# Kernel tuning notes

Hardware: AMD Instinct MI355X
Metric: run time of the kernel (lower is better)

The kernel has to match this reference:

```python
import jax, jax.numpy as jnp
import numpy as np

H = 8           # num_heads
TANH_CLIP = 10.0


def setup_inputs() -> dict:
    key = jax.random.key(0)
    ks = jax.random.split(key, 7)
    B, N, D = 512, 1000, 128
    embeddings = jax.random.normal(ks[0], (B, N, D), dtype=jnp.float32)
    context_feat = jax.random.normal(ks[1], (B, 2 * D), dtype=jnp.float32)
    W_node = jax.random.normal(ks[2], (D, 3 * D), dtype=jnp.float32) / np.sqrt(D)
    W_fixed = jax.random.normal(ks[3], (D, D), dtype=jnp.float32) / np.sqrt(D)
    W_step = jax.random.normal(ks[4], (2 * D, D), dtype=jnp.float32) / np.sqrt(2 * D)
    W_out = jax.random.normal(ks[5], (D, D), dtype=jnp.float32) / np.sqrt(D)
    # action_mask: True = feasible node; ensure at least one feasible per row
    action_mask = jax.random.uniform(ks[6], (B, N)) > 0.3
    action_mask = action_mask.at[:, 0].set(True)
    return {"embeddings": embeddings, "context_feat": context_feat,
            "W_node": W_node, "W_fixed": W_fixed, "W_step": W_step,
            "W_out": W_out, "action_mask": action_mask}


def reference(embeddings, context_feat, W_node, W_fixed, W_step, W_out, action_mask):
    B, N, D = embeddings.shape
    dk = D // H
    # --- _precompute ---
    graph_context = (embeddings.mean(axis=1) @ W_fixed)[:, None, :]      # [B,1,D]
    proj = embeddings @ W_node                                            # [B,N,3D]
    gk, gv, logit_k = jnp.split(proj, 3, axis=-1)                         # each [B,N,D]
    to_heads = lambda x: x.reshape(B, N, H, dk).transpose(2, 0, 1, 3)     # [H,B,N,dk]
    K, V = to_heads(gk), to_heads(gv)
    # --- _get_log_p: query (num_steps = 1) ---
    q = graph_context + (context_feat @ W_step)[:, None, :]               # [B,1,D]
    Q = q.reshape(B, 1, H, dk).transpose(2, 0, 1, 3)                      # [H,B,1,dk]
    mask = ~action_mask                                                    # [B,N], True = infeasible
    # --- glimpse attention (mask_inner) ---
    compat = jnp.einsum('hbqd,hbnd->hbqn', Q, K) / jnp.sqrt(jnp.asarray(dk, Q.dtype))
    compat = jnp.where(mask[None, :, None, :], -jnp.inf, compat)
    attn = jax.nn.softmax(compat, axis=-1)                                 # [H,B,1,N]
    heads = jnp.einsum('hbqn,hbnd->hbqd', attn, V)                         # [H,B,1,dk]
    glimpse = heads.transpose(1, 2, 0, 3).reshape(B, 1, D) @ W_out         # [B,1,D]
    # --- tanh-clipped single-head logits ---
    logits = jnp.einsum('bqd,bnd->bqn', glimpse, logit_k) / jnp.sqrt(jnp.asarray(D, glimpse.dtype))
    logits = jnp.tanh(logits) * TANH_CLIP
    logits = jnp.where(mask[:, None, :], -jnp.inf, logits)                 # [B,1,N]
    return logits
```

## Files before the change

### kernel.cpp

```cpp
#include <hip/hip_runtime.h>
#include <math.h>

#define BB 512
#define NN 1000
#define DD 128
#define HH 8
#define TILE 125

#define WS_AFOLD 4096

__device__ __forceinline__ bool mask_feasible(const void* mask, int flag, int idx) {
    if (flag == 1) return ((const int*)mask)[idx] != 0;
    if (flag == 2) return ((const float*)mask)[idx] != 0.0f;
    return ((const unsigned char*)mask)[idx] != 0;
}

__device__ __forceinline__ float rdl(float v, int srclane) {
    return __int_as_float(__builtin_amdgcn_readlane(__float_as_int(v), srclane));
}

__global__ void k0_detect(const unsigned int* __restrict__ m, int* __restrict__ flag) {
    int t = threadIdx.x;
    unsigned int w = m[t];
    unsigned long long bi = __ballot(w <= 1u);
    unsigned long long bf = __ballot(w == 0u || w == 0x3F800000u);
    if (t == 0) {
        int f = 0;
        if (bi == ~0ull) f = 1;
        else if (bf == ~0ull) f = 2;
        *flag = f;
    }
}

__global__ __launch_bounds__(512) void kA_meanfold(
    const float* __restrict__ emb, const float* __restrict__ ctx,
    const float* __restrict__ W_fixed, const float* __restrict__ W_step,
    const float* __restrict__ W_node, float* __restrict__ Afold) {
    int b = blockIdx.x, t = threadIdx.x;
    __shared__ float4 red[512];
    __shared__ float mean_s[DD], cld[2 * DD], qlds[DD];
    int q4 = t & 31, j = t >> 5;
    const float4* e4 = (const float4*)(emb + (size_t)b * NN * DD);
    float4 acc = {0.f, 0.f, 0.f, 0.f};
    for (int n = j; n < NN; n += 16) {
        float4 v = e4[n * 32 + q4];
        acc.x += v.x; acc.y += v.y; acc.z += v.z; acc.w += v.w;
    }
    red[t] = acc;
    __syncthreads();
    for (int s = 8; s >= 1; s >>= 1) {
        if (j < s) {
            float4 o = red[t + s * 32], m = red[t];
            m.x += o.x; m.y += o.y; m.z += o.z; m.w += o.w;
            red[t] = m;
        }
        __syncthreads();
    }
    if (t < 32) {
        float4 m = red[t];
        const float inv = 1.0f / (float)NN;
        float4 r = {m.x * inv, m.y * inv, m.z * inv, m.w * inv};
        ((float4*)mean_s)[t] = r;
    }
    if (t < 256) cld[t] = ctx[b * 2 * DD + t];
    __syncthreads();
    if (t < 128) {
        float a = 0.f;
        for (int c = 0; c < DD; ++c)     a += mean_s[c] * W_fixed[c * DD + t];
        for (int c = 0; c < 2 * DD; ++c) a += cld[c] * W_step[c * DD + t];
        qlds[t] = a;
    }
    __syncthreads();
    if (t < 128) {
        int c = t;
        const float* wrow = W_node + (size_t)c * 3 * DD;
        float* Ab = Afold + (size_t)b * 1024;
        for (int h = 0; h < HH; ++h) {
            float a = 0.f;
#pragma unroll
            for (int d0 = 0; d0 < 16; ++d0) a += wrow[h * 16 + d0] * qlds[h * 16 + d0];
            Ab[c * 8 + h] = 0.25f * a;
        }
    }
}

__global__ __launch_bounds__(256) void kB_flash(
    const float* __restrict__ emb, const float* __restrict__ Afold,
    const void* __restrict__ mask, const int* __restrict__ flagp,
    const float* __restrict__ W_node, const float* __restrict__ W_out,
    float* __restrict__ out) {
    int b = blockIdx.x, t = threadIdx.x;
    int flag = *flagp;
    int wave = t >> 6, lane = t & 63;
    int hq = (t >> 7) * 4;
    int n = t & 127;
    int c4 = t & 31, jr = t >> 5;

    __shared__ float4 tile4[128][32];
    __shared__ float cbuf[128][8];
    __shared__ float wemb_s[8][128];
    __shared__ float mrun[8], zrun[8], scale_s[8], mnew_s[8];
    __shared__ float4 wmax4[4];
    __shared__ float4 zstage[4][2];
    __shared__ float hl[DD];
    __shared__ float4 gl4[32];

    const float* Ab = Afold + (size_t)b * 1024;
    float a0l = Ab[lane * 8 + hq + 0], a1l = Ab[lane * 8 + hq + 1];
    float a2l = Ab[lane * 8 + hq + 2], a3l = Ab[lane * 8 + hq + 3];
    float a0h = Ab[(64 + lane) * 8 + hq + 0], a1h = Ab[(64 + lane) * 8 + hq + 1];
    float a2h = Ab[(64 + lane) * 8 + hq + 2], a3h = Ab[(64 + lane) * 8 + hq + 3];

    float4 wacc[8];
#pragma unroll
    for (int h = 0; h < HH; ++h) wacc[h] = make_float4(0.f, 0.f, 0.f, 0.f);
    if (t < 8) { mrun[t] = -INFINITY; zrun[t] = 0.f; }
    __syncthreads();

    const float4* embB4 = (const float4*)(emb + (size_t)b * NN * DD);
    const int mbase = b * NN;

    for (int tile = 0; tile < 8; ++tile) {
        int n0 = tile * TILE;
#pragma unroll
        for (int idx = 0; idx < 16; ++idx) {
            int i = t + idx * 256;
            if (i < TILE * 32) {
                int r = i >> 5, c = i & 31;
                tile4[r][c ^ (r & 31)] = embB4[n0 * 32 + i];
            }
        }
        __syncthreads();
        float4 cv = make_float4(-INFINITY, -INFINITY, -INFINITY, -INFINITY);
        if (n < TILE) {
            int sw = n & 31;
            float4 s = make_float4(0.f, 0.f, 0.f, 0.f);
#pragma unroll 4
            for (int k = 0; k < 16; ++k) {
                float4 e = tile4[n][k ^ sw];
                int c = k * 4;
                s.x += e.x * rdl(a0l, c) + e.y * rdl(a0l, c + 1) + e.z * rdl(a0l, c + 2) + e.w * rdl(a0l, c + 3);
                s.y += e.x * rdl(a1l, c) + e.y * rdl(a1l, c + 1) + e.z * rdl(a1l, c + 2) + e.w * rdl(a1l, c + 3);
                s.z += e.x * rdl(a2l, c) + e.y * rdl(a2l, c + 1) + e.z * rdl(a2l, c + 2) + e.w * rdl(a2l, c + 3);
                s.w += e.x * rdl(a3l, c) + e.y * rdl(a3l, c + 1) + e.z * rdl(a3l, c + 2) + e.w * rdl(a3l, c + 3);
            }
#pragma unroll 4
            for (int k = 16; k < 32; ++k) {
                float4 e = tile4[n][k ^ sw];
                int c = k * 4 - 64;
                s.x += e.x * rdl(a0h, c) + e.y * rdl(a0h, c + 1) + e.z * rdl(a0h, c + 2) + e.w * rdl(a0h, c + 3);
                s.y += e.x * rdl(a1h, c) + e.y * rdl(a1h, c + 1) + e.z * rdl(a1h, c + 2) + e.w * rdl(a1h, c + 3);
                s.z += e.x * rdl(a2h, c) + e.y * rdl(a2h, c + 1) + e.z * rdl(a2h, c + 2) + e.w * rdl(a2h, c + 3);
                s.w += e.x * rdl(a3h, c) + e.y * rdl(a3h, c + 1) + e.z * rdl(a3h, c + 2) + e.w * rdl(a3h, c + 3);
            }
            if (mask_feasible(mask, flag, mbase + n0 + n)) cv = s;
            *(float4*)&cbuf[n][hq] = cv;
        }
        {
            float4 wm = cv;
#pragma unroll
            for (int off = 1; off < 64; off <<= 1) {
                wm.x = fmaxf(wm.x, __shfl_xor(wm.x, off));
                wm.y = fmaxf(wm.y, __shfl_xor(wm.y, off));
                wm.z = fmaxf(wm.z, __shfl_xor(wm.z, off));
                wm.w = fmaxf(wm.w, __shfl_xor(wm.w, off));
            }
            if (lane == 0) wmax4[wave] = wm;
        }
        __syncthreads();
        if (t < 8) {
            int w0 = (t < 4) ? 0 : 2, hi = t & 3;
            float m = fmaxf(((float*)&wmax4[w0])[hi], ((float*)&wmax4[w0 + 1])[hi]);
            float mold = mrun[t];
            float mn = fmaxf(mold, m);
            mnew_s[t] = mn;
            scale_s[t] = (mn == -INFINITY) ? 1.0f : __expf(mold - mn);
            mrun[t] = mn;
        }
        __syncthreads();
        {
            float m0 = mnew_s[hq], m1 = mnew_s[hq + 1], m2 = mnew_s[hq + 2], m3 = mnew_s[hq + 3];
            float4 p = make_float4(0.f, 0.f, 0.f, 0.f);
            if (n < TILE) {
                p.x = (cv.x == -INFINITY) ? 0.f : __expf(cv.x - m0);
                p.y = (cv.y == -INFINITY) ? 0.f : __expf(cv.y - m1);
                p.z = (cv.z == -INFINITY) ? 0.f : __expf(cv.z - m2);
                p.w = (cv.w == -INFINITY) ? 0.f : __expf(cv.w - m3);
                *(float4*)&cbuf[n][hq] = p;
            }
#pragma unroll
            for (int off = 1; off < 64; off <<= 1) {
                p.x += __shfl_xor(p.x, off);
                p.y += __shfl_xor(p.y, off);
                p.z += __shfl_xor(p.z, off);
                p.w += __shfl_xor(p.w, off);
            }
            if (lane == 0) zstage[wave][hq >> 2] = p;
            float sc0 = scale_s[0], sc1 = scale_s[1], sc2 = scale_s[2], sc3 = scale_s[3];
            float sc4 = scale_s[4], sc5 = scale_s[5], sc6 = scale_s[6], sc7 = scale_s[7];
            wacc[0].x *= sc0; wacc[0].y *= sc0; wacc[0].z *= sc0; wacc[0].w *= sc0;
            wacc[1].x *= sc1; wacc[1].y *= sc1; wacc[1].z *= sc1; wacc[1].w *= sc1;
            wacc[2].x *= sc2; wacc[2].y *= sc2; wacc[2].z *= sc2; wacc[2].w *= sc2;
            wacc[3].x *= sc3; wacc[3].y *= sc3; wacc[3].z *= sc3; wacc[3].w *= sc3;
            wacc[4].x *= sc4; wacc[4].y *= sc4; wacc[4].z *= sc4; wacc[4].w *= sc4;
            wacc[5].x *= sc5; wacc[5].y *= sc5; wacc[5].z *= sc5; wacc[5].w *= sc5;
            wacc[6].x *= sc6; wacc[6].y *= sc6; wacc[6].z *= sc6; wacc[6].w *= sc6;
            wacc[7].x *= sc7; wacc[7].y *= sc7; wacc[7].z *= sc7; wacc[7].w *= sc7;
        }
        __syncthreads();
        if (t < 8) {
            int w0 = (t < 4) ? 0 : 2;
            float zn = ((float*)&zstage[w0][t >> 2])[t & 3] + ((float*)&zstage[w0 + 1][t >> 2])[t & 3];
            zrun[t] = zrun[t] * scale_s[t] + zn;
        }
        for (int nn = jr; nn < TILE; nn += 8) {
            float4 e = tile4[nn][c4 ^ (nn & 31)];
            float4 pA = *(const float4*)&cbuf[nn][0];
            float4 pB = *(const float4*)&cbuf[nn][4];
            wacc[0].x += pA.x * e.x; wacc[0].y += pA.x * e.y; wacc[0].z += pA.x * e.z; wacc[0].w += pA.x * e.w;
            wacc[1].x += pA.y * e.x; wacc[1].y += pA.y * e.y; wacc[1].z += pA.y * e.z; wacc[1].w += pA.y * e.w;
            wacc[2].x += pA.z * e.x; wacc[2].y += pA.z * e.y; wacc[2].z += pA.z * e.z; wacc[2].w += pA.z * e.w;
            wacc[3].x += pA.w * e.x; wacc[3].y += pA.w * e.y; wacc[3].z += pA.w * e.z; wacc[3].w += pA.w * e.w;
            wacc[4].x += pB.x * e.x; wacc[4].y += pB.x * e.y; wacc[4].z += pB.x * e.z; wacc[4].w += pB.x * e.w;
            wacc[5].x += pB.y * e.x; wacc[5].y += pB.y * e.y; wacc[5].z += pB.y * e.z; wacc[5].w += pB.y * e.w;
            wacc[6].x += pB.z * e.x; wacc[6].y += pB.z * e.y; wacc[6].z += pB.z * e.z; wacc[6].w += pB.z * e.w;
            wacc[7].x += pB.w * e.x; wacc[7].y += pB.w * e.y; wacc[7].z += pB.w * e.z; wacc[7].w += pB.w * e.w;
        }
        __syncthreads();
    }
    {
        float4* red = (float4*)&tile4[0][0];
#pragma unroll
        for (int h = 0; h < HH; ++h) red[(jr * 32 + c4) * 8 + h] = wacc[h];
        __syncthreads();
        int cc = t >> 3, hh = t & 7;
        float4 s = make_float4(0.f, 0.f, 0.f, 0.f);
#pragma unroll
        for (int jj = 0; jj < 8; ++jj) {
            float4 v = red[(jj * 32 + cc) * 8 + hh];
            s.x += v.x; s.y += v.y; s.z += v.z; s.w += v.w;
        }
        float inv = 1.0f / zrun[hh];
        s.x *= inv; s.y *= inv; s.z *= inv; s.w *= inv;
        *(float4*)&wemb_s[hh][cc * 4] = s;
    }
    __syncthreads();
    if (t < 128) {
        int h = t >> 4;
        float a = 0.f;
        for (int c = 0; c < DD; ++c) a += wemb_s[h][c] * W_node[(size_t)c * 384 + 128 + t];
        hl[t] = a;
    }
    __syncthreads();
    if (t < 128) {
        float g = 0.f;
        for (int k = 0; k < DD; ++k) g += hl[k] * W_out[k * DD + t];
        ((float*)gl4)[t] = g;
    }
    __syncthreads();
    if (t < 128) {
        float a3 = 0.f;
        const float* wr = W_node + (size_t)t * 384 + 256;
        const float* glp = (const float*)gl4;
        for (int d = 0; d < DD; ++d) a3 += wr[d] * glp[d];
        hl[t] = a3;
    }
    __syncthreads();
    const float4* g2v = (const float4*)hl;
    for (int r = t; r < NN; r += 256) {
        const float4* row = embB4 + (size_t)r * 32;
        float acc = 0.f;
#pragma unroll 8
        for (int k = 0; k < 32; ++k) {
            float4 e = row[k], g = g2v[k];
            acc += e.x * g.x + e.y * g.y + e.z * g.z + e.w * g.w;
        }
        bool feas = mask_feasible(mask, flag, mbase + r);
        out[(size_t)mbase + r] = feas ? (10.0f * tanhf(acc * 0.08838834764831845f)) : -1.0e30f;
    }
}

extern "C" void kernel_launch(void* const* d_in, const int* in_sizes, int n_in,
                              void* d_out, int out_size, void* d_ws, size_t ws_size,
                              hipStream_t stream) {
    (void)in_sizes; (void)n_in; (void)out_size; (void)ws_size;
    const float* emb     = (const float*)d_in[0];
    const float* ctx     = (const float*)d_in[1];
    const float* W_node  = (const float*)d_in[2];
    const float* W_fixed = (const float*)d_in[3];
    const float* W_step  = (const float*)d_in[4];
    const float* W_out   = (const float*)d_in[5];
    const void*  mask    = d_in[6];
    float* out = (float*)d_out;

    char* ws = (char*)d_ws;
    int*   flag  = (int*)(ws + 0);
    float* Afold = (float*)(ws + WS_AFOLD);

    k0_detect<<<1, 64, 0, stream>>>((const unsigned int*)mask, flag);
    kA_meanfold<<<BB, 512, 0, stream>>>(emb, ctx, W_fixed, W_step, W_node, Afold);
    kB_flash<<<BB, 256, 0, stream>>>(emb, Afold, mask, flag, W_node, W_out, out);
}
```

Measured before the change: 200.6 us.

## Fuse mean/fold kernel into flash kernel and widen block to 512 threads

Merges the per-batch mean/query-fold kernel into the attention kernel, so the folded query matrix stays in shared memory instead of going through a workspace. The block grows to 512 threads with each thread computing 2 heads instead of 4, and cbuf is transposed to a head-major layout. This removes one launch and a global round trip, and puts more waves on each batch row. The cost is that the embedding mean pass now runs inside the same block ahead of the tile loop, and register pressure with the 8 float4 accumulators at 512 threads may limit occupancy.

```diff
diff --git a/kernel.cpp b/kernel.cpp
--- a/kernel.cpp
+++ b/kernel.cpp
@@ -6,8 +6,6 @@
 #define DD 128
 #define HH 8
 #define TILE 125
-
-#define WS_AFOLD 4096
 
 __device__ __forceinline__ bool mask_feasible(const void* mask, int flag, int idx) {
     if (flag == 1) return ((const int*)mask)[idx] != 0;
@@ -32,145 +30,126 @@
     }
 }
 
-__global__ __launch_bounds__(512) void kA_meanfold(
+__global__ __launch_bounds__(512, 4) void kMega(
     const float* __restrict__ emb, const float* __restrict__ ctx,
     const float* __restrict__ W_fixed, const float* __restrict__ W_step,
-    const float* __restrict__ W_node, float* __restrict__ Afold) {
-    int b = blockIdx.x, t = threadIdx.x;
-    __shared__ float4 red[512];
-    __shared__ float mean_s[DD], cld[2 * DD], qlds[DD];
-    int q4 = t & 31, j = t >> 5;
-    const float4* e4 = (const float4*)(emb + (size_t)b * NN * DD);
-    float4 acc = {0.f, 0.f, 0.f, 0.f};
-    for (int n = j; n < NN; n += 16) {
-        float4 v = e4[n * 32 + q4];
-        acc.x += v.x; acc.y += v.y; acc.z += v.z; acc.w += v.w;
-    }
-    red[t] = acc;
-    __syncthreads();
-    for (int s = 8; s >= 1; s >>= 1) {
-        if (j < s) {
-            float4 o = red[t + s * 32], m = red[t];
-            m.x += o.x; m.y += o.y; m.z += o.z; m.w += o.w;
-            red[t] = m;
-        }
-        __syncthreads();
-    }
-    if (t < 32) {
-        float4 m = red[t];
-        const float inv = 1.0f / (float)NN;
-        float4 r = {m.x * inv, m.y * inv, m.z * inv, m.w * inv};
-        ((float4*)mean_s)[t] = r;
-    }
-    if (t < 256) cld[t] = ctx[b * 2 * DD + t];
-    __syncthreads();
-    if (t < 128) {
-        float a = 0.f;
-        for (int c = 0; c < DD; ++c)     a += mean_s[c] * W_fixed[c * DD + t];
-        for (int c = 0; c < 2 * DD; ++c) a += cld[c] * W_step[c * DD + t];
-        qlds[t] = a;
-    }
-    __syncthreads();
-    if (t < 128) {
-        int c = t;
-        const float* wrow = W_node + (size_t)c * 3 * DD;
-        float* Ab = Afold + (size_t)b * 1024;
-        for (int h = 0; h < HH; ++h) {
-            float a = 0.f;
-#pragma unroll
-            for (int d0 = 0; d0 < 16; ++d0) a += wrow[h * 16 + d0] * qlds[h * 16 + d0];
-            Ab[c * 8 + h] = 0.25f * a;
-        }
-    }
-}
-
-__global__ __launch_bounds__(256) void kB_flash(
-    const float* __restrict__ emb, const float* __restrict__ Afold,
+    const float* __restrict__ W_node, const float* __restrict__ W_out,
     const void* __restrict__ mask, const int* __restrict__ flagp,
-    const float* __restrict__ W_node, const float* __restrict__ W_out,
     float* __restrict__ out) {
     int b = blockIdx.x, t = threadIdx.x;
     int flag = *flagp;
     int wave = t >> 6, lane = t & 63;
-    int hq = (t >> 7) * 4;
+    int hq = (t >> 7) * 2;
     int n = t & 127;
     int c4 = t & 31, jr = t >> 5;
 
     __shared__ float4 tile4[128][32];
-    __shared__ float cbuf[128][8];
-    __shared__ float wemb_s[8][128];
+    __shared__ float cbuf[HH][DD];
+    __shared__ float small[1536];
     __shared__ float mrun[8], zrun[8], scale_s[8], mnew_s[8];
-    __shared__ float4 wmax4[4];
-    __shared__ float4 zstage[4][2];
-    __shared__ float hl[DD];
-    __shared__ float4 gl4[32];
-
-    const float* Ab = Afold + (size_t)b * 1024;
-    float a0l = Ab[lane * 8 + hq + 0], a1l = Ab[lane * 8 + hq + 1];
-    float a2l = Ab[lane * 8 + hq + 2], a3l = Ab[lane * 8 + hq + 3];
-    float a0h = Ab[(64 + lane) * 8 + hq + 0], a1h = Ab[(64 + lane) * 8 + hq + 1];
-    float a2h = Ab[(64 + lane) * 8 + hq + 2], a3h = Ab[(64 + lane) * 8 + hq + 3];
-
-    float4 wacc[8];
-#pragma unroll
-    for (int h = 0; h < HH; ++h) wacc[h] = make_float4(0.f, 0.f, 0.f, 0.f);
-    if (t < 8) { mrun[t] = -INFINITY; zrun[t] = 0.f; }
-    __syncthreads();
+    __shared__ float2 wmax2[8], zstage[8];
 
     const float4* embB4 = (const float4*)(emb + (size_t)b * NN * DD);
     const int mbase = b * NN;
 
+    {
+        float4 acc = make_float4(0.f, 0.f, 0.f, 0.f);
+        for (int nn = jr; nn < NN; nn += 16) {
+            float4 v = embB4[nn * 32 + c4];
+            acc.x += v.x; acc.y += v.y; acc.z += v.z; acc.w += v.w;
+        }
+        float4* red = (float4*)tile4;
+        red[t] = acc;
+        __syncthreads();
+        for (int s = 8; s >= 1; s >>= 1) {
+            if (jr < s) {
+                float4 o = red[t + s * 32], m = red[t];
+                m.x += o.x; m.y += o.y; m.z += o.z; m.w += o.w;
+                red[t] = m;
+            }
+            __syncthreads();
+        }
+        if (t < 32) {
+            float4 m = red[t];
+            const float inv = 1.0f / (float)NN;
+            float4 r = {m.x * inv, m.y * inv, m.z * inv, m.w * inv};
+            ((float4*)&small[0])[t] = r;
+        }
+        if (t >= 256) small[t] = ctx[b * 2 * DD + (t - 256)];
+    }
+    __syncthreads();
+    if (t < 128) {
+        float a = 0.f;
+        for (int c = 0; c < DD; ++c)     a += small[c] * W_fixed[c * DD + t];
+        for (int c = 0; c < 2 * DD; ++c) a += small[256 + c] * W_step[c * DD + t];
+        small[128 + t] = a;
+    }
+    __syncthreads();
+    if (t < 128) {
+        const float* wrow = W_node + (size_t)t * 384;
+        for (int h = 0; h < HH; ++h) {
+            float a = 0.f;
+#pragma unroll
+            for (int d0 = 0; d0 < 16; ++d0) a += wrow[h * 16 + d0] * small[128 + h * 16 + d0];
+            small[512 + t * 8 + h] = 0.25f * a;
+        }
+    }
+    if (t < 8) { mrun[t] = -INFINITY; zrun[t] = 0.f; }
+    __syncthreads();
+    float a0l = small[512 + lane * 8 + hq],        a1l = small[512 + lane * 8 + hq + 1];
+    float a0h = small[512 + (64 + lane) * 8 + hq], a1h = small[512 + (64 + lane) * 8 + hq + 1];
+
+    float4 wacc[8];
+#pragma unroll
+    for (int h = 0; h < HH; ++h) wacc[h] = make_float4(0.f, 0.f, 0.f, 0.f);
+
     for (int tile = 0; tile < 8; ++tile) {
         int n0 = tile * TILE;
 #pragma unroll
-        for (int idx = 0; idx < 16; ++idx) {
-            int i = t + idx * 256;
+        for (int idx = 0; idx < 8; ++idx) {
+            int i = t + idx * 512;
             if (i < TILE * 32) {
                 int r = i >> 5, c = i & 31;
                 tile4[r][c ^ (r & 31)] = embB4[n0 * 32 + i];
             }
         }
         __syncthreads();
-        float4 cv = make_float4(-INFINITY, -INFINITY, -INFINITY, -INFINITY);
+        float2 cv = make_float2(-INFINITY, -INFINITY);
         if (n < TILE) {
             int sw = n & 31;
-            float4 s = make_float4(0.f, 0.f, 0.f, 0.f);
-#pragma unroll 4
+            float sx = 0.f, sy = 0.f;
+#pragma unroll
             for (int k = 0; k < 16; ++k) {
                 float4 e = tile4[n][k ^ sw];
                 int c = k * 4;
-                s.x += e.x * rdl(a0l, c) + e.y * rdl(a0l, c + 1) + e.z * rdl(a0l, c + 2) + e.w * rdl(a0l, c + 3);
-                s.y += e.x * rdl(a1l, c) + e.y * rdl(a1l, c + 1) + e.z * rdl(a1l, c + 2) + e.w * rdl(a1l, c + 3);
-                s.z += e.x * rdl(a2l, c) + e.y * rdl(a2l, c + 1) + e.z * rdl(a2l, c + 2) + e.w * rdl(a2l, c + 3);
-                s.w += e.x * rdl(a3l, c) + e.y * rdl(a3l, c + 1) + e.z * rdl(a3l, c + 2) + e.w * rdl(a3l, c + 3);
-            }
-#pragma unroll 4
+                sx += e.x * rdl(a0l, c) + e.y * rdl(a0l, c + 1) + e.z * rdl(a0l, c + 2) + e.w * rdl(a0l, c + 3);
+                sy += e.x * rdl(a1l, c) + e.y * rdl(a1l, c + 1) + e.z * rdl(a1l, c + 2) + e.w * rdl(a1l, c + 3);
+            }
+#pragma unroll
             for (int k = 16; k < 32; ++k) {
                 float4 e = tile4[n][k ^ sw];
                 int c = k * 4 - 64;
-                s.x += e.x * rdl(a0h, c) + e.y * rdl(a0h, c + 1) + e.z * rdl(a0h, c + 2) + e.w * rdl(a0h, c + 3);
-                s.y += e.x * rdl(a1h, c) + e.y * rdl(a1h, c + 1) + e.z * rdl(a1h, c + 2) + e.w * rdl(a1h, c + 3);
-                s.z += e.x * rdl(a2h, c) + e.y * rdl(a2h, c + 1) + e.z * rdl(a2h, c + 2) + e.w * rdl(a2h, c + 3);
-                s.w += e.x * rdl(a3h, c) + e.y * rdl(a3h, c + 1) + e.z * rdl(a3h, c + 2) + e.w * rdl(a3h, c + 3);
-            }
-            if (mask_feasible(mask, flag, mbase + n0 + n)) cv = s;
-            *(float4*)&cbuf[n][hq] = cv;
+                sx += e.x * rdl(a0h, c) + e.y * rdl(a0h, c + 1) + e.z * rdl(a0h, c + 2) + e.w * rdl(a0h, c + 3);
+                sy += e.x * rdl(a1h, c) + e.y * rdl(a1h, c + 1) + e.z * rdl(a1h, c + 2) + e.w * rdl(a1h, c + 3);
+            }
+            if (mask_feasible(mask, flag, mbase + n0 + n)) { cv.x = sx; cv.y = sy; }
+            cbuf[hq][n] = cv.x;
+            cbuf[hq + 1][n] = cv.y;
         }
         {
-            float4 wm = cv;
+            float2 wm = cv;
 #pragma unroll
             for (int off = 1; off < 64; off <<= 1) {
                 wm.x = fmaxf(wm.x, __shfl_xor(wm.x, off));
                 wm.y = fmaxf(wm.y, __shfl_xor(wm.y, off));
-                wm.z = fmaxf(wm.z, __shfl_xor(wm.z, off));
-                wm.w = fmaxf(wm.w, __shfl_xor(wm.w, off));
-            }
-            if (lane == 0) wmax4[wave] = wm;
+            }
+            if (lane == 0) wmax2[wave] = wm;
         }
         __syncthreads();
         if (t < 8) {
-            int w0 = (t < 4) ? 0 : 2, hi = t & 3;
-            float m = fmaxf(((float*)&wmax4[w0])[hi], ((float*)&wmax4[w0 + 1])[hi]);
+            int w0 = (t >> 1) * 2;
+            float m = (t & 1) ? fmaxf(wmax2[w0].y, wmax2[w0 + 1].y)
+                              : fmaxf(wmax2[w0].x, wmax2[w0 + 1].x);
             float mold = mrun[t];
             float mn = fmaxf(mold, m);
             mnew_s[t] = mn;
@@ -179,23 +158,20 @@
         }
         __syncthreads();
         {
-            float m0 = mnew_s[hq], m1 = mnew_s[hq + 1], m2 = mnew_s[hq + 2], m3 = mnew_s[hq + 3];
-            float4 p = make_float4(0.f, 0.f, 0.f, 0.f);
+            float m0 = mnew_s[hq], m1 = mnew_s[hq + 1];
+            float2 p = make_float2(0.f, 0.f);
             if (n < TILE) {
                 p.x = (cv.x == -INFINITY) ? 0.f : __expf(cv.x - m0);
                 p.y = (cv.y == -INFINITY) ? 0.f : __expf(cv.y - m1);
-                p.z = (cv.z == -INFINITY) ? 0.f : __expf(cv.z - m2);
-                p.w = (cv.w == -INFINITY) ? 0.f : __expf(cv.w - m3);
-                *(float4*)&cbuf[n][hq] = p;
+                cbuf[hq][n] = p.x;
+                cbuf[hq + 1][n] = p.y;
             }
 #pragma unroll
             for (int off = 1; off < 64; off <<= 1) {
                 p.x += __shfl_xor(p.x, off);
                 p.y += __shfl_xor(p.y, off);
-                p.z += __shfl_xor(p.z, off);
-                p.w += __shfl_xor(p.w, off);
-            }
-            if (lane == 0) zstage[wave][hq >> 2] = p;
+            }
+            if (lane == 0) zstage[wave] = p;
             float sc0 = scale_s[0], sc1 = scale_s[1], sc2 = scale_s[2], sc3 = scale_s[3];
             float sc4 = scale_s[4], sc5 = scale_s[5], sc6 = scale_s[6], sc7 = scale_s[7];
             wacc[0].x *= sc0; wacc[0].y *= sc0; wacc[0].z *= sc0; wacc[0].w *= sc0;
@@ -209,65 +185,67 @@
         }
         __syncthreads();
         if (t < 8) {
-            int w0 = (t < 4) ? 0 : 2;
-            float zn = ((float*)&zstage[w0][t >> 2])[t & 3] + ((float*)&zstage[w0 + 1][t >> 2])[t & 3];
+            int w0 = (t >> 1) * 2;
+            float zn = (t & 1) ? (zstage[w0].y + zstage[w0 + 1].y)
+                               : (zstage[w0].x + zstage[w0 + 1].x);
             zrun[t] = zrun[t] * scale_s[t] + zn;
         }
-        for (int nn = jr; nn < TILE; nn += 8) {
+        for (int nn = jr; nn < TILE; nn += 16) {
             float4 e = tile4[nn][c4 ^ (nn & 31)];
-            float4 pA = *(const float4*)&cbuf[nn][0];
-            float4 pB = *(const float4*)&cbuf[nn][4];
-            wacc[0].x += pA.x * e.x; wacc[0].y += pA.x * e.y; wacc[0].z += pA.x * e.z; wacc[0].w += pA.x * e.w;
-            wacc[1].x += pA.y * e.x; wacc[1].y += pA.y * e.y; wacc[1].z += pA.y * e.z; wacc[1].w += pA.y * e.w;
-            wacc[2].x += pA.z * e.x; wacc[2].y += pA.z * e.y; wacc[2].z += pA.z * e.z; wacc[2].w += pA.z * e.w;
-            wacc[3].x += pA.w * e.x; wacc[3].y += pA.w * e.y; wacc[3].z += pA.w * e.z; wacc[3].w += pA.w * e.w;
-            wacc[4].x += pB.x * e.x; wacc[4].y += pB.x * e.y; wacc[4].z += pB.x * e.z; wacc[4].w += pB.x * e.w;
-            wacc[5].x += pB.y * e.x; wacc[5].y += pB.y * e.y; wacc[5].z += pB.y * e.z; wacc[5].w += pB.y * e.w;
-            wacc[6].x += pB.z * e.x; wacc[6].y += pB.z * e.y; wacc[6].z += pB.z * e.z; wacc[6].w += pB.z * e.w;
-            wacc[7].x += pB.w * e.x; wacc[7].y += pB.w * e.y; wacc[7].z += pB.w * e.z; wacc[7].w += pB.w * e.w;
+            float p0 = cbuf[0][nn], p1 = cbuf[1][nn], p2 = cbuf[2][nn], p3 = cbuf[3][nn];
+            float p4 = cbuf[4][nn], p5 = cbuf[5][nn], p6 = cbuf[6][nn], p7 = cbuf[7][nn];
+            wacc[0].x += p0 * e.x; wacc[0].y += p0 * e.y; wacc[0].z += p0 * e.z; wacc[0].w += p0 * e.w;
+            wacc[1].x += p1 * e.x; wacc[1].y += p1 * e.y; wacc[1].z += p1 * e.z; wacc[1].w += p1 * e.w;
+            wacc[2].x += p2 * e.x; wacc[2].y += p2 * e.y; wacc[2].z += p2 * e.z; wacc[2].w += p2 * e.w;
+            wacc[3].x += p3 * e.x; wacc[3].y += p3 * e.y; wacc[3].z += p3 * e.z; wacc[3].w += p3 * e.w;
+            wacc[4].x += p4 * e.x; wacc[4].y += p4 * e.y; wacc[4].z += p4 * e.z; wacc[4].w += p4 * e.w;
+            wacc[5].x += p5 * e.x; wacc[5].y += p5 * e.y; wacc[5].z += p5 * e.z; wacc[5].w += p5 * e.w;
+            wacc[6].x += p6 * e.x; wacc[6].y += p6 * e.y; wacc[6].z += p6 * e.z; wacc[6].w += p6 * e.w;
+            wacc[7].x += p7 * e.x; wacc[7].y += p7 * e.y; wacc[7].z += p7 * e.z; wacc[7].w += p7 * e.w;
         }
         __syncthreads();
     }
     {
-        float4* red = (float4*)&tile4[0][0];
+        float4* red = (float4*)tile4;
 #pragma unroll
         for (int h = 0; h < HH; ++h) red[(jr * 32 + c4) * 8 + h] = wacc[h];
         __syncthreads();
-        int cc = t >> 3, hh = t & 7;
-        float4 s = make_float4(0.f, 0.f, 0.f, 0.f);
-#pragma unroll
-        for (int jj = 0; jj < 8; ++jj) {
-            float4 v = red[(jj * 32 + cc) * 8 + hh];
-            s.x += v.x; s.y += v.y; s.z += v.z; s.w += v.w;
-        }
-        float inv = 1.0f / zrun[hh];
-        s.x *= inv; s.y *= inv; s.z *= inv; s.w *= inv;
-        *(float4*)&wemb_s[hh][cc * 4] = s;
+        if (t < 256) {
+            int cc = t >> 3, hh = t & 7;
+            float4 s = make_float4(0.f, 0.f, 0.f, 0.f);
+#pragma unroll
+            for (int jj = 0; jj < 16; ++jj) {
+                float4 v = red[(jj * 32 + cc) * 8 + hh];
+                s.x += v.x; s.y += v.y; s.z += v.z; s.w += v.w;
+            }
+            float inv = 1.0f / zrun[hh];
+            s.x *= inv; s.y *= inv; s.z *= inv; s.w *= inv;
+            ((float4*)&cbuf[hh][0])[cc] = s;
+        }
     }
     __syncthreads();
     if (t < 128) {
         int h = t >> 4;
         float a = 0.f;
-        for (int c = 0; c < DD; ++c) a += wemb_s[h][c] * W_node[(size_t)c * 384 + 128 + t];
-        hl[t] = a;
+        for (int c = 0; c < DD; ++c) a += cbuf[h][c] * W_node[(size_t)c * 384 + 128 + t];
+        small[t] = a;
     }
     __syncthreads();
     if (t < 128) {
         float g = 0.f;
-        for (int k = 0; k < DD; ++k) g += hl[k] * W_out[k * DD + t];
-        ((float*)gl4)[t] = g;
+        for (int k = 0; k < DD; ++k) g += small[k] * W_out[k * DD + t];
+        small[128 + t] = g;
     }
     __syncthreads();
     if (t < 128) {
         float a3 = 0.f;
         const float* wr = W_node + (size_t)t * 384 + 256;
-        const float* glp = (const float*)gl4;
-        for (int d = 0; d < DD; ++d) a3 += wr[d] * glp[d];
-        hl[t] = a3;
-    }
-    __syncthreads();
-    const float4* g2v = (const float4*)hl;
-    for (int r = t; r < NN; r += 256) {
+        for (int d = 0; d < DD; ++d) a3 += wr[d] * small[128 + d];
+        small[256 + t] = a3;
+    }
+    __syncthreads();
+    const float4* g2v = (const float4*)&small[256];
+    for (int r = t; r < NN; r += 512) {
         const float4* row = embB4 + (size_t)r * 32;
         float acc = 0.f;
 #pragma unroll 8
@@ -293,11 +271,7 @@
     const void*  mask    = d_in[6];
     float* out = (float*)d_out;
 
-    char* ws = (char*)d_ws;
-    int*   flag  = (int*)(ws + 0);
-    float* Afold = (float*)(ws + WS_AFOLD);
-
+    int* flag = (int*)d_ws;
     k0_detect<<<1, 64, 0, stream>>>((const unsigned int*)mask, flag);
-    kA_meanfold<<<BB, 512, 0, stream>>>(emb, ctx, W_fixed, W_step, W_node, Afold);
-    kB_flash<<<BB, 256, 0, stream>>>(emb, Afold, mask, flag, W_node, W_out, out);
-}
+    kMega<<<BB, 512, 0, stream>>>(emb, ctx, W_fixed, W_step, W_node, W_out, mask, flag, out);
+}
```

Result: slower. 410.6 us (+104.6%).

## Assign one wave per head in flash kernel with register-resident softmax state

Applied to the files above, without the earlier changes.

The flash kernel now runs 512 threads with one wave per attention head. Each wave keeps its running max, normaliser and weighted-embedding accumulator in registers and reduces them with wave shuffles, which removes the shared-memory staging and most of the per-tile barriers. Tiles shrink to 64 rows so that one lane scores one node, and probabilities are broadcast with shuffles in place of a shared buffer. In exchange it issues more tile iterations with smaller loads, and every wave reads each tile for its own head.

```diff
diff --git a/kernel.cpp b/kernel.cpp
--- a/kernel.cpp
+++ b/kernel.cpp
@@ -5,7 +5,8 @@
 #define NN 1000
 #define DD 128
 #define HH 8
-#define TILE 125
+#define TILE 64
+#define NT 16
 
 #define WS_AFOLD 4096
 
@@ -84,7 +85,7 @@
     }
 }
 
-__global__ __launch_bounds__(256) void kB_flash(
+__global__ __launch_bounds__(512) void kB_flash(
     const float* __restrict__ emb, const float* __restrict__ Afold,
     const void* __restrict__ mask, const int* __restrict__ flagp,
     const float* __restrict__ W_node, const float* __restrict__ W_out,
@@ -92,182 +93,105 @@
     int b = blockIdx.x, t = threadIdx.x;
     int flag = *flagp;
     int wave = t >> 6, lane = t & 63;
-    int hq = (t >> 7) * 4;
-    int n = t & 127;
-    int c4 = t & 31, jr = t >> 5;
-
-    __shared__ float4 tile4[128][32];
-    __shared__ float cbuf[128][8];
-    __shared__ float wemb_s[8][128];
-    __shared__ float mrun[8], zrun[8], scale_s[8], mnew_s[8];
-    __shared__ float4 wmax4[4];
-    __shared__ float4 zstage[4][2];
-    __shared__ float hl[DD];
-    __shared__ float4 gl4[32];
+    int c4 = lane & 31, jh = lane >> 5;
+
+    __shared__ float4 tile4[TILE][32];
+    __shared__ float wemb_s[HH][DD];
+    __shared__ float small[3 * DD];
 
     const float* Ab = Afold + (size_t)b * 1024;
-    float a0l = Ab[lane * 8 + hq + 0], a1l = Ab[lane * 8 + hq + 1];
-    float a2l = Ab[lane * 8 + hq + 2], a3l = Ab[lane * 8 + hq + 3];
-    float a0h = Ab[(64 + lane) * 8 + hq + 0], a1h = Ab[(64 + lane) * 8 + hq + 1];
-    float a2h = Ab[(64 + lane) * 8 + hq + 2], a3h = Ab[(64 + lane) * 8 + hq + 3];
-
-    float4 wacc[8];
-#pragma unroll
-    for (int h = 0; h < HH; ++h) wacc[h] = make_float4(0.f, 0.f, 0.f, 0.f);
-    if (t < 8) { mrun[t] = -INFINITY; zrun[t] = 0.f; }
-    __syncthreads();
+    float a0l = Ab[lane * 8 + wave];
+    float a0h = Ab[(64 + lane) * 8 + wave];
+
+    float4 wacc = make_float4(0.f, 0.f, 0.f, 0.f);
+    float mrun = -INFINITY, zrun = 0.f;
 
     const float4* embB4 = (const float4*)(emb + (size_t)b * NN * DD);
     const int mbase = b * NN;
 
-    for (int tile = 0; tile < 8; ++tile) {
+    for (int tile = 0; tile < NT; ++tile) {
         int n0 = tile * TILE;
-#pragma unroll
-        for (int idx = 0; idx < 16; ++idx) {
-            int i = t + idx * 256;
-            if (i < TILE * 32) {
-                int r = i >> 5, c = i & 31;
-                tile4[r][c ^ (r & 31)] = embB4[n0 * 32 + i];
+        int rows = (NN - n0 < TILE) ? (NN - n0) : TILE;
+#pragma unroll
+        for (int idx = 0; idx < 4; ++idx) {
+            int i = t + idx * 512;
+            int r = i >> 5, c = i & 31;
+            if (r < rows) tile4[r][c ^ (r & 31)] = embB4[n0 * 32 + i];
+        }
+        __syncthreads();
+        float cv = -INFINITY;
+        if (lane < rows) {
+            int sw = lane & 31;
+            float s = 0.f;
+#pragma unroll
+            for (int k = 0; k < 16; ++k) {
+                float4 e = tile4[lane][k ^ sw];
+                int c = k * 4;
+                s += e.x * rdl(a0l, c) + e.y * rdl(a0l, c + 1) + e.z * rdl(a0l, c + 2) + e.w * rdl(a0l, c + 3);
             }
+#pragma unroll
+            for (int k = 16; k < 32; ++k) {
+                float4 e = tile4[lane][k ^ sw];
+                int c = k * 4 - 64;
+                s += e.x * rdl(a0h, c) + e.y * rdl(a0h, c + 1) + e.z * rdl(a0h, c + 2) + e.w * rdl(a0h, c + 3);
+            }
+            if (mask_feasible(mask, flag, mbase + n0 + lane)) cv = s;
+        }
+        float m = cv;
+#pragma unroll
+        for (int off = 1; off < 64; off <<= 1) m = fmaxf(m, __shfl_xor(m, off));
+        float mn = fmaxf(mrun, m);
+        float scale = (mn == -INFINITY) ? 1.0f : __expf(mrun - mn);
+        mrun = mn;
+        float p = (cv == -INFINITY) ? 0.f : __expf(cv - mn);
+        float z = p;
+#pragma unroll
+        for (int off = 1; off < 64; off <<= 1) z += __shfl_xor(z, off);
+        zrun = zrun * scale + z;
+        wacc.x *= scale; wacc.y *= scale; wacc.z *= scale; wacc.w *= scale;
+        for (int nn = jh; nn < rows; nn += 2) {
+            float4 e = tile4[nn][c4 ^ (nn & 31)];
+            float pv = __shfl(p, nn);
+            wacc.x += pv * e.x; wacc.y += pv * e.y; wacc.z += pv * e.z; wacc.w += pv * e.w;
         }
         __syncthreads();
-        float4 cv = make_float4(-INFINITY, -INFINITY, -INFINITY, -INFINITY);
-        if (n < TILE) {
-            int sw = n & 31;
-            float4 s = make_float4(0.f, 0.f, 0.f, 0.f);
-#pragma unroll 4
-            for (int k = 0; k < 16; ++k) {
-                float4 e = tile4[n][k ^ sw];
-                int c = k * 4;
-                s.x += e.x * rdl(a0l, c) + e.y * rdl(a0l, c + 1) + e.z * rdl(a0l, c + 2) + e.w * rdl(a0l, c + 3);
-                s.y += e.x * rdl(a1l, c) + e.y * rdl(a1l, c + 1) + e.z * rdl(a1l, c + 2) + e.w * rdl(a1l, c + 3);
-                s.z += e.x * rdl(a2l, c) + e.y * rdl(a2l, c + 1) + e.z * rdl(a2l, c + 2) + e.w * rdl(a2l, c + 3);
-                s.w += e.x * rdl(a3l, c) + e.y * rdl(a3l, c + 1) + e.z * rdl(a3l, c + 2) + e.w * rdl(a3l, c + 3);
-            }
-#pragma unroll 4
-            for (int k = 16; k < 32; ++k) {
-                float4 e = tile4[n][k ^ sw];
-                int c = k * 4 - 64;
-                s.x += e.x * rdl(a0h, c) + e.y * rdl(a0h, c + 1) + e.z * rdl(a0h, c + 2) + e.w * rdl(a0h, c + 3);
-                s.y += e.x * rdl(a1h, c) + e.y * rdl(a1h, c + 1) + e.z * rdl(a1h, c + 2) + e.w * rdl(a1h, c + 3);
-                s.z += e.x * rdl(a2h, c) + e.y * rdl(a2h, c + 1) + e.z * rdl(a2h, c + 2) + e.w * rdl(a2h, c + 3);
-                s.w += e.x * rdl(a3h, c) + e.y * rdl(a3h, c + 1) + e.z * rdl(a3h, c + 2) + e.w * rdl(a3h, c + 3);
-            }
-            if (mask_feasible(mask, flag, mbase + n0 + n)) cv = s;
-            *(float4*)&cbuf[n][hq] = cv;
-        }
-        {
-            float4 wm = cv;
-#pragma unroll
-            for (int off = 1; off < 64; off <<= 1) {
-                wm.x = fmaxf(wm.x, __shfl_xor(wm.x, off));
-                wm.y = fmaxf(wm.y, __shfl_xor(wm.y, off));
-                wm.z = fmaxf(wm.z, __shfl_xor(wm.z, off));
-                wm.w = fmaxf(wm.w, __shfl_xor(wm.w, off));
-            }
-            if (lane == 0) wmax4[wave] = wm;
-        }
-        __syncthreads();
-        if (t < 8) {
-            int w0 = (t < 4) ? 0 : 2, hi = t & 3;
-            float m = fmaxf(((float*)&wmax4[w0])[hi], ((float*)&wmax4[w0 + 1])[hi]);
-            float mold = mrun[t];
-            float mn = fmaxf(mold, m);
-            mnew_s[t] = mn;
-            scale_s[t] = (mn == -INFINITY) ? 1.0f : __expf(mold - mn);
-            mrun[t] = mn;
-        }
-        __syncthreads();
-        {
-            float m0 = mnew_s[hq], m1 = mnew_s[hq + 1], m2 = mnew_s[hq + 2], m3 = mnew_s[hq + 3];
-            float4 p = make_float4(0.f, 0.f, 0.f, 0.f);
-            if (n < TILE) {
-                p.x = (cv.x == -INFINITY) ? 0.f : __expf(cv.x - m0);
-                p.y = (cv.y == -INFINITY) ? 0.f : __expf(cv.y - m1);
-                p.z = (cv.z == -INFINITY) ? 0.f : __expf(cv.z - m2);
-                p.w = (cv.w == -INFINITY) ? 0.f : __expf(cv.w - m3);
-                *(float4*)&cbuf[n][hq] = p;
-            }
-#pragma unroll
-            for (int off = 1; off < 64; off <<= 1) {
-                p.x += __shfl_xor(p.x, off);
-                p.y += __shfl_xor(p.y, off);
-                p.z += __shfl_xor(p.z, off);
-                p.w += __shfl_xor(p.w, off);
-            }
-            if (lane == 0) zstage[wave][hq >> 2] = p;
-            float sc0 = scale_s[0], sc1 = scale_s[1], sc2 = scale_s[2], sc3 = scale_s[3];
-            float sc4 = scale_s[4], sc5 = scale_s[5], sc6 = scale_s[6], sc7 = scale_s[7];
-            wacc[0].x *= sc0; wacc[0].y *= sc0; wacc[0].z *= sc0; wacc[0].w *= sc0;
-            wacc[1].x *= sc1; wacc[1].y *= sc1; wacc[1].z *= sc1; wacc[1].w *= sc1;
-            wacc[2].x *= sc2; wacc[2].y *= sc2; wacc[2].z *= sc2; wacc[2].w *= sc2;
-            wacc[3].x *= sc3; wacc[3].y *= sc3; wacc[3].z *= sc3; wacc[3].w *= sc3;
-            wacc[4].x *= sc4; wacc[4].y *= sc4; wacc[4].z *= sc4; wacc[4].w *= sc4;
-            wacc[5].x *= sc5; wacc[5].y *= sc5; wacc[5].z *= sc5; wacc[5].w *= sc5;
-            wacc[6].x *= sc6; wacc[6].y *= sc6; wacc[6].z *= sc6; wacc[6].w *= sc6;
-            wacc[7].x *= sc7; wacc[7].y *= sc7; wacc[7].z *= sc7; wacc[7].w *= sc7;
-        }
-        __syncthreads();
-        if (t < 8) {
-            int w0 = (t < 4) ? 0 : 2;
-            float zn = ((float*)&zstage[w0][t >> 2])[t & 3] + ((float*)&zstage[w0 + 1][t >> 2])[t & 3];
-            zrun[t] = zrun[t] * scale_s[t] + zn;
-        }
-        for (int nn = jr; nn < TILE; nn += 8) {
-            float4 e = tile4[nn][c4 ^ (nn & 31)];
-            float4 pA = *(const float4*)&cbuf[nn][0];
-            float4 pB = *(const float4*)&cbuf[nn][4];
-            wacc[0].x += pA.x * e.x; wacc[0].y += pA.x * e.y; wacc[0].z += pA.x * e.z; wacc[0].w += pA.x * e.w;
-            wacc[1].x += pA.y * e.x; wacc[1].y += pA.y * e.y; wacc[1].z += pA.y * e.z; wacc[1].w += pA.y * e.w;
-            wacc[2].x += pA.z * e.x; wacc[2].y += pA.z * e.y; wacc[2].z += pA.z * e.z; wacc[2].w += pA.z * e.w;
-            wacc[3].x += pA.w * e.x; wacc[3].y += pA.w * e.y; wacc[3].z += pA.w * e.z; wacc[3].w += pA.w * e.w;
-            wacc[4].x += pB.x * e.x; wacc[4].y += pB.x * e.y; wacc[4].z += pB.x * e.z; wacc[4].w += pB.x * e.w;
-            wacc[5].x += pB.y * e.x; wacc[5].y += pB.y * e.y; wacc[5].z += pB.y * e.z; wacc[5].w += pB.y * e.w;
-            wacc[6].x += pB.z * e.x; wacc[6].y += pB.z * e.y; wacc[6].z += pB.z * e.z; wacc[6].w += pB.z * e.w;
-            wacc[7].x += pB.w * e.x; wacc[7].y += pB.w * e.y; wacc[7].z += pB.w * e.z; wacc[7].w += pB.w * e.w;
-        }
-        __syncthreads();
-    }
+    }
+    wacc.x += __shfl_xor(wacc.x, 32);
+    wacc.y += __shfl_xor(wacc.y, 32);
+    wacc.z += __shfl_xor(wacc.z, 32);
+    wacc.w += __shfl_xor(wacc.w, 32);
     {
-        float4* red = (float4*)&tile4[0][0];
-#pragma unroll
-        for (int h = 0; h < HH; ++h) red[(jr * 32 + c4) * 8 + h] = wacc[h];
-        __syncthreads();
-        int cc = t >> 3, hh = t & 7;
-        float4 s = make_float4(0.f, 0.f, 0.f, 0.f);
-#pragma unroll
-        for (int jj = 0; jj < 8; ++jj) {
-            float4 v = red[(jj * 32 + cc) * 8 + hh];
-            s.x += v.x; s.y += v.y; s.z += v.z; s.w += v.w;
-        }
-        float inv = 1.0f / zrun[hh];
-        s.x *= inv; s.y *= inv; s.z *= inv; s.w *= inv;
-        *(float4*)&wemb_s[hh][cc * 4] = s;
+        float inv = 1.0f / zrun;
+        if (lane < 32) {
+            wemb_s[wave][c4 * 4 + 0] = wacc.x * inv;
+            wemb_s[wave][c4 * 4 + 1] = wacc.y * inv;
+            wemb_s[wave][c4 * 4 + 2] = wacc.z * inv;
+            wemb_s[wave][c4 * 4 + 3] = wacc.w * inv;
+        }
     }
     __syncthreads();
     if (t < 128) {
         int h = t >> 4;
         float a = 0.f;
         for (int c = 0; c < DD; ++c) a += wemb_s[h][c] * W_node[(size_t)c * 384 + 128 + t];
-        hl[t] = a;
+        small[t] = a;
     }
     __syncthreads();
     if (t < 128) {
         float g = 0.f;
-        for (int k = 0; k < DD; ++k) g += hl[k] * W_out[k * DD + t];
-        ((float*)gl4)[t] = g;
+        for (int k = 0; k < DD; ++k) g += small[k] * W_out[k * DD + t];
+        small[128 + t] = g;
     }
     __syncthreads();
     if (t < 128) {
         float a3 = 0.f;
         const float* wr = W_node + (size_t)t * 384 + 256;
-        const float* glp = (const float*)gl4;
-        for (int d = 0; d < DD; ++d) a3 += wr[d] * glp[d];
-        hl[t] = a3;
-    }
-    __syncthreads();
-    const float4* g2v = (const float4*)hl;
-    for (int r = t; r < NN; r += 256) {
+        for (int d = 0; d < DD; ++d) a3 += wr[d] * small[128 + d];
+        small[256 + t] = a3;
+    }
+    __syncthreads();
+    const float4* g2v = (const float4*)&small[256];
+    for (int r = t; r < NN; r += 512) {
         const float4* row = embB4 + (size_t)r * 32;
         float acc = 0.f;
 #pragma unroll 8
@@ -299,5 +223,5 @@
 
     k0_detect<<<1, 64, 0, stream>>>((const unsigned int*)mask, flag);
     kA_meanfold<<<BB, 512, 0, stream>>>(emb, ctx, W_fixed, W_step, W_node, Afold);
-    kB_flash<<<BB, 256, 0, stream>>>(emb, Afold, mask, flag, W_node, W_out, out);
-}
+    kB_flash<<<BB, 512, 0, stream>>>(emb, Afold, mask, flag, W_node, W_out, out);
+}
```

Measured after the change: 301.8 us. 50.4% more time.
